# Optimization experiments

Hardware: AMD Instinct MI355X
Metric: run time of the kernel (lower is better)

The kernel has to match this reference:

```python
import jax, jax.numpy as jnp
import numpy as np

N = 100000
E = 1600000
IN_DIM, HID, Z = 128, 64, 32


def gcn_conv(x, src, dst, num_nodes, W, b):
    """PyG GCNConv: add self-loops, symmetric deg^-1/2 normalization.
    x: [N, F_in]; src/dst: [E] int (self-loops already appended by caller wrapper).
    """
    h = x @ W  # [N, F_out] transform first (PyG order)
    ones = jnp.ones(src.shape[0], dtype=x.dtype)
    deg = jax.ops.segment_sum(ones, dst, num_segments=num_nodes)  # in-degree incl. self-loop
    dinv = jnp.where(deg > 0, jax.lax.rsqrt(deg), 0.0)
    norm = dinv[src] * dinv[dst]  # [E]
    msgs = h[src] * norm[:, None]  # [E, F_out] irregular gather
    out = jax.ops.segment_sum(msgs, dst, num_segments=num_nodes)  # scatter-add
    return out + b


def setup_inputs() -> dict:
    key = jax.random.key(0)
    ks = jax.random.split(key, 10)
    x = jax.random.normal(ks[0], (N, IN_DIM), dtype=jnp.float32)
    edge_index = jax.random.randint(ks[1], (2, E), 0, N, dtype=jnp.int64)

    def glorot(k, fan_in, fan_out):
        s = jnp.sqrt(6.0 / (fan_in + fan_out))
        return jax.random.uniform(k, (fan_in, fan_out), jnp.float32, -s, s)

    return {
        "x": x,
        "edge_index": edge_index,
        "W1": glorot(ks[2], IN_DIM, HID),
        "b1": jnp.zeros((HID,), jnp.float32),
        "W2": glorot(ks[3], HID, Z),
        "b2": jnp.zeros((Z,), jnp.float32),
        "Wmu": glorot(ks[4], Z, Z),
        "bmu": jnp.zeros((Z,), jnp.float32),
        "Wlv": glorot(ks[5], Z, Z),
        "blv": jnp.zeros((Z,), jnp.float32),
    }


def reference(x, edge_index, W1, b1, W2, b2, Wmu, bmu, Wlv, blv):
    num_nodes = x.shape[0]
    loop = jnp.arange(num_nodes, dtype=edge_index.dtype)
    src = jnp.concatenate([edge_index[0], loop])  # self-loops appended
    dst = jnp.concatenate([edge_index[1], loop])
    h = jax.nn.relu(gcn_conv(x, src, dst, num_nodes, W1, b1))
    h = gcn_conv(h, src, dst, num_nodes, W2, b2)
    mu = h @ Wmu + bmu
    logvar = h @ Wlv + blv
    return (mu, logvar)
```

## Files before the change

kernel.cpp:

```cpp
#include <hip/hip_runtime.h>

#define N_NODES 100000
#define N_EDGES 1600000
#define IN_F   128
#define HID_F  64
#define Z_F    32
#define NBUK   782
#define BCAP   3072
#define P1T    4096
#define P1_BLOCKS ((N_EDGES + P1T - 1) / P1T)
#define AGG_CAP 2048
#define G1_BLOCKS ((N_NODES + 63) / 64)

typedef unsigned int uint32;
typedef __attribute__((ext_vector_type(8))) short bf16x8;
typedef __attribute__((ext_vector_type(4))) float f32x4;

__device__ __forceinline__ unsigned short f2bf(float f) {
    unsigned u = __float_as_uint(f);
    u = (u + 0x7FFF + ((u >> 16) & 1)) >> 16;
    return (unsigned short)u;
}
__device__ __forceinline__ uint32 pack2bf(float lo, float hi) {
    return (uint32)f2bf(lo) | ((uint32)f2bf(hi) << 16);
}
__device__ __forceinline__ float bflo(uint32 u) { return __uint_as_float(u << 16); }
__device__ __forceinline__ float bfhi(uint32 u) { return __uint_as_float(u & 0xFFFF0000u); }

#define ACC8(u) { a0 += bflo(u.x); a1 += bfhi(u.x); a2 += bflo(u.y); a3 += bfhi(u.y); \
                  a4 += bflo(u.z); a5 += bfhi(u.z); a6 += bflo(u.w); a7 += bfhi(u.w); }

__global__ __launch_bounds__(512) void phase1_kernel(const int* __restrict__ ei,
                                                     int* __restrict__ gcur,
                                                     uint32* __restrict__ pairs,
                                                     const float* __restrict__ W1,
                                                     const float* __restrict__ W2,
                                                     const float* __restrict__ Wmu,
                                                     const float* __restrict__ Wlv,
                                                     unsigned short* __restrict__ Wt1,
                                                     unsigned short* __restrict__ Wt2,
                                                     unsigned short* __restrict__ Wth) {
    if (blockIdx.x == P1_BLOCKS) {
        int t = threadIdx.x;
        for (int i = t; i < IN_F * HID_F; i += 512) {
            int n = i >> 7, k = i & 127;
            Wt1[i] = f2bf(W1[k * HID_F + n]);
        }
        for (int i = t; i < HID_F * Z_F; i += 512) {
            int n = i >> 6, k = i & 63;
            Wt2[i] = f2bf(W2[k * Z_F + n]);
        }
        for (int i = t; i < Z_F * 64; i += 512) {
            int n = i >> 5, k = i & 31;
            Wth[i] = f2bf(n < 32 ? Wmu[k * Z_F + n] : Wlv[k * Z_F + (n - 32)]);
        }
        return;
    }
    __shared__ int hist[NBUK];
    __shared__ int lbase[NBUK];
    __shared__ int gbase[NBUK];
    __shared__ int lcur[NBUK];
    __shared__ uint32 stage[P1T];
    __shared__ unsigned short sbid[P1T];
    __shared__ int part[512];
    int tid = threadIdx.x;
    int e0 = blockIdx.x * P1T;
    int ecnt = N_EDGES - e0; if (ecnt > P1T) ecnt = P1T;
    for (int b = tid; b < NBUK; b += 512) { hist[b] = 0; lcur[b] = 0; }
    __syncthreads();
    int myd[8];
#pragma unroll
    for (int i = 0; i < 8; i++) {
        int k = tid + i * 512;
        myd[i] = (k < ecnt) ? ei[N_EDGES + e0 + k] : -1;
    }
#pragma unroll
    for (int i = 0; i < 8; i++)
        if (myd[i] >= 0) atomicAdd(&hist[myd[i] >> 7], 1);
    __syncthreads();
    int t2 = tid * 2;
    int l0 = 0, l1 = 0, s = 0;
    if (t2 + 0 < NBUK) { l0 = hist[t2 + 0]; s += l0; }
    if (t2 + 1 < NBUK) { l1 = hist[t2 + 1]; s += l1; }
    part[tid] = s;
    __syncthreads();
    for (int off = 1; off < 512; off <<= 1) {
        int add = (tid >= off) ? part[tid - off] : 0;
        __syncthreads();
        part[tid] += add;
        __syncthreads();
    }
    int run = part[tid] - s;
    if (t2 + 0 < NBUK) { lbase[t2 + 0] = run; run += l0; }
    if (t2 + 1 < NBUK) { lbase[t2 + 1] = run; }
    for (int b = tid; b < NBUK; b += 512) {
        int h = hist[b];
        gbase[b] = h ? atomicAdd(&gcur[b], h) : 0;
    }
    __syncthreads();
#pragma unroll
    for (int i = 0; i < 8; i++) {
        int k = tid + i * 512;
        if (k < ecnt) {
            int sN = ei[e0 + k];
            int d  = myd[i];
            int b = d >> 7;
            int slot = lbase[b] + atomicAdd(&lcur[b], 1);
            stage[slot] = (uint32)sN | ((uint32)(d & 127) << 17);
            sbid[slot] = (unsigned short)b;
        }
    }
    __syncthreads();
    for (int k = tid; k < ecnt; k += 512) {
        int b = sbid[k];
        int r = gbase[b] + (k - lbase[k < ecnt ? b : 0]);
        r = gbase[b] + (k - lbase[b]);
        if (r < BCAP) pairs[(size_t)b * BCAP + r] = stage[k];
    }
}

__global__ __launch_bounds__(256) void p2g1_kernel(const uint32* __restrict__ pairs,
                                                   const int* __restrict__ gcur,
                                                   int* __restrict__ rowptr,
                                                   float* __restrict__ dinv,
                                                   int* __restrict__ col,
                                                   const float* __restrict__ x,
                                                   const unsigned short* __restrict__ Wt1,
                                                   unsigned short* __restrict__ t1) {
    int tid = threadIdx.x;
    if (blockIdx.x < NBUK) {
        __shared__ int lhist[128];
        __shared__ int lscan[128];
        __shared__ int lcur[128];
        __shared__ int stage[BCAP];
        __shared__ int wsum[4];
        int b = blockIdx.x;
        int cnt_b = gcur[b];
        if (cnt_b > BCAP) cnt_b = BCAP;
        int partial = 0;
        for (int i = tid; i < b; i += 256) partial += gcur[i];
#pragma unroll
        for (int off = 32; off > 0; off >>= 1) partial += __shfl_down(partial, off);
        if (tid < 128) { lhist[tid] = 0; lcur[tid] = 0; }
        if ((tid & 63) == 0) wsum[tid >> 6] = partial;
        __syncthreads();
        int gbase = wsum[0] + wsum[1] + wsum[2] + wsum[3];
        int node0 = b << 7;
        int nb = N_NODES - node0;
        if (nb > 128) nb = 128;
        const uint32* pb = pairs + (size_t)b * BCAP;
        for (int k = tid; k < cnt_b; k += 256) atomicAdd(&lhist[pb[k] >> 17], 1);
        __syncthreads();
        int v = (tid < 128) ? lhist[tid] : 0;
        if (tid < 128) lscan[tid] = v;
        __syncthreads();
        for (int off = 1; off < 128; off <<= 1) {
            int add = (tid < 128 && tid >= off) ? lscan[tid - off] : 0;
            __syncthreads();
            if (tid < 128) lscan[tid] += add;
            __syncthreads();
        }
        if (tid < 128) lscan[tid] -= v;
        __syncthreads();
        if (tid < nb) {
            rowptr[node0 + tid] = gbase + lscan[tid];
            dinv[node0 + tid] = rsqrtf((float)(lhist[tid] + 1));
        }
        if (b == NBUK - 1 && tid == 0) rowptr[N_NODES] = N_EDGES;
        for (int k = tid; k < cnt_b; k += 256) {
            uint32 u = pb[k];
            int ld = u >> 17;
            int r = atomicAdd(&lcur[ld], 1);
            stage[lscan[ld] + r] = (int)(u & 0x1FFFF);
        }
        __syncthreads();
        for (int k = tid; k < cnt_b; k += 256) col[gbase + k] = stage[k];
        return;
    }
    __shared__ unsigned short Cs[64 * 72];
    __shared__ float dv[64];
    __shared__ int h64[64];
    int g = blockIdx.x - NBUK;
    int node0 = g * 64;
    int bk = node0 >> 7, half = (node0 >> 6) & 1;
    int cnt_b = gcur[bk];
    if (cnt_b > BCAP) cnt_b = BCAP;
    if (tid < 64) h64[tid] = 0;
    __syncthreads();
    const uint32* pb = pairs + (size_t)bk * BCAP;
    for (int k = tid; k < cnt_b; k += 256) {
        int ld = pb[k] >> 17;
        if ((ld >> 6) == half) atomicAdd(&h64[ld & 63], 1);
    }
    __syncthreads();
    if (tid < 64) {
        int n = node0 + tid;
        dv[tid] = (n < N_NODES) ? rsqrtf((float)(h64[tid] + 1)) : 0.f;
    }
    __syncthreads();
    int w = tid >> 6, lane = tid & 63;
    int m = lane & 15, quad = lane >> 4;
    int row = w * 16 + m;
    int node = node0 + row;
    const float* xr = x + (size_t)min(node, N_NODES - 1) * IN_F;
    f32x4 acc0 = {0.f, 0.f, 0.f, 0.f};
    f32x4 acc1 = acc0, acc2 = acc0, acc3 = acc0;
#pragma unroll
    for (int ks = 0; ks < 4; ks++) {
        int kb = ks * 32 + quad * 8;
        float4 f0 = *(const float4*)(xr + kb);
        float4 f1 = *(const float4*)(xr + kb + 4);
        union { bf16x8 v; unsigned short u[8]; } A;
        A.u[0] = f2bf(f0.x); A.u[1] = f2bf(f0.y); A.u[2] = f2bf(f0.z); A.u[3] = f2bf(f0.w);
        A.u[4] = f2bf(f1.x); A.u[5] = f2bf(f1.y); A.u[6] = f2bf(f1.z); A.u[7] = f2bf(f1.w);
        bf16x8 b0 = *(const bf16x8*)&Wt1[(0 * 16 + m) * IN_F + kb];
        bf16x8 b1 = *(const bf16x8*)&Wt1[(1 * 16 + m) * IN_F + kb];
        bf16x8 b2 = *(const bf16x8*)&Wt1[(2 * 16 + m) * IN_F + kb];
        bf16x8 b3 = *(const bf16x8*)&Wt1[(3 * 16 + m) * IN_F + kb];
        acc0 = __builtin_amdgcn_mfma_f32_16x16x32_bf16(A.v, b0, acc0, 0, 0, 0);
        acc1 = __builtin_amdgcn_mfma_f32_16x16x32_bf16(A.v, b1, acc1, 0, 0, 0);
        acc2 = __builtin_amdgcn_mfma_f32_16x16x32_bf16(A.v, b2, acc2, 0, 0, 0);
        acc3 = __builtin_amdgcn_mfma_f32_16x16x32_bf16(A.v, b3, acc3, 0, 0, 0);
    }
    int rbase = w * 16 + quad * 4;
#pragma unroll
    for (int reg = 0; reg < 4; reg++) {
        int r = rbase + reg;
        float d = dv[r];
        Cs[r * 72 +  0 + m] = f2bf(acc0[reg] * d);
        Cs[r * 72 + 16 + m] = f2bf(acc1[reg] * d);
        Cs[r * 72 + 32 + m] = f2bf(acc2[reg] * d);
        Cs[r * 72 + 48 + m] = f2bf(acc3[reg] * d);
    }
    __syncthreads();
#pragma unroll
    for (int it = 0; it < 4; it++) {
        int idx = it * 256 + tid;
        int r = idx >> 4, c = idx & 15;
        int nd = node0 + r;
        if (nd < N_NODES) {
            uint2 vv = *(const uint2*)&Cs[r * 72 + c * 4];
            *(uint2*)&t1[(size_t)nd * HID_F + c * 4] = vv;
        }
    }
}

__global__ __launch_bounds__(256) void agg1gemm2_kernel(const unsigned short* __restrict__ t1,
                                                        const int* __restrict__ rowptr,
                                                        const int* __restrict__ col,
                                                        const float* __restrict__ dinv,
                                                        const float* __restrict__ b1,
                                                        const unsigned short* __restrict__ Wt2,
                                                        unsigned short* __restrict__ t2s) {
    __shared__ int lcol[AGG_CAP];
    __shared__ int lrp[65];
    __shared__ float ldv[64];
    __shared__ unsigned short h1s[64 * 72];
    __shared__ unsigned short Cs[64 * 36];
    int tid = threadIdx.x;
    int node0 = blockIdx.x * 64;
    if (tid < 65) lrp[tid] = rowptr[min(node0 + tid, N_NODES)];
    __syncthreads();
    int s0 = lrp[0];
    int cnt = lrp[64] - s0; if (cnt > AGG_CAP) cnt = AGG_CAP;
    for (int k = tid; k < cnt; k += 256) lcol[k] = col[s0 + k];
    if (tid < 64) {
        int n = node0 + tid;
        ldv[tid] = (n < N_NODES) ? dinv[n] : 0.f;
    }
    __syncthreads();
    int lane = tid & 63, w = tid >> 6;
    int grp = lane >> 3, fl = lane & 7;
    int gg = w * 8 + grp;
    const uint4* t1q = (const uint4*)t1;
    float4 bb0 = ((const float4*)b1)[fl * 2];
    float4 bb1 = ((const float4*)b1)[fl * 2 + 1];
#pragma unroll
    for (int rep = 0; rep < 2; rep++) {
        int li = gg + rep * 32;
        int node = node0 + li;
        uint4 pk = make_uint4(0u, 0u, 0u, 0u);
        if (node < N_NODES) {
            int s = lrp[li] - s0;
            int e = lrp[li + 1] - s0; if (e > cnt) e = cnt;
            float a0 = 0.f, a1 = 0.f, a2 = 0.f, a3 = 0.f;
            float a4 = 0.f, a5 = 0.f, a6 = 0.f, a7 = 0.f;
            int p = s;
            for (; p + 3 < e; p += 4) {
                int c0 = lcol[p], c1 = lcol[p + 1], c2 = lcol[p + 2], c3 = lcol[p + 3];
                uint4 u0 = t1q[(size_t)c0 * 8 + fl];
                uint4 u1 = t1q[(size_t)c1 * 8 + fl];
                uint4 u2 = t1q[(size_t)c2 * 8 + fl];
                uint4 u3 = t1q[(size_t)c3 * 8 + fl];
                ACC8(u0); ACC8(u1); ACC8(u2); ACC8(u3);
            }
            for (; p < e; p++) {
                uint4 u = t1q[(size_t)lcol[p] * 8 + fl];
                ACC8(u);
            }
            uint4 us = t1q[(size_t)node * 8 + fl];
            float di = ldv[li];
            float o0 = fmaxf(di * (a0 + bflo(us.x)) + bb0.x, 0.f);
            float o1 = fmaxf(di * (a1 + bfhi(us.x)) + bb0.y, 0.f);
            float o2 = fmaxf(di * (a2 + bflo(us.y)) + bb0.z, 0.f);
            float o3 = fmaxf(di * (a3 + bfhi(us.y)) + bb0.w, 0.f);
            float o4 = fmaxf(di * (a4 + bflo(us.z)) + bb1.x, 0.f);
            float o5 = fmaxf(di * (a5 + bfhi(us.z)) + bb1.y, 0.f);
            float o6 = fmaxf(di * (a6 + bflo(us.w)) + bb1.z, 0.f);
            float o7 = fmaxf(di * (a7 + bfhi(us.w)) + bb1.w, 0.f);
            pk.x = pack2bf(o0, o1);
            pk.y = pack2bf(o2, o3);
            pk.z = pack2bf(o4, o5);
            pk.w = pack2bf(o6, o7);
        }
        *(uint4*)&h1s[li * 72 + fl * 8] = pk;
    }
    __syncthreads();
    int m = lane & 15, quad = lane >> 4;
    int row = w * 16 + m;
    f32x4 acc0 = {0.f, 0.f, 0.f, 0.f};
    f32x4 acc1 = acc0;
#pragma unroll
    for (int ks = 0; ks < 2; ks++) {
        int kb = ks * 32 + quad * 8;
        bf16x8 a  = *(const bf16x8*)&h1s[row * 72 + kb];
        bf16x8 b0 = *(const bf16x8*)&Wt2[(0 * 16 + m) * HID_F + kb];
        bf16x8 b1v = *(const bf16x8*)&Wt2[(1 * 16 + m) * HID_F + kb];
        acc0 = __builtin_amdgcn_mfma_f32_16x16x32_bf16(a, b0, acc0, 0, 0, 0);
        acc1 = __builtin_amdgcn_mfma_f32_16x16x32_bf16(a, b1v, acc1, 0, 0, 0);
    }
    int rbase = w * 16 + quad * 4;
#pragma unroll
    for (int reg = 0; reg < 4; reg++) {
        int r = rbase + reg;
        float d = ldv[r];
        Cs[r * 36 +  0 + m] = f2bf(acc0[reg] * d);
        Cs[r * 36 + 16 + m] = f2bf(acc1[reg] * d);
    }
    __syncthreads();
#pragma unroll
    for (int it = 0; it < 2; it++) {
        int idx = it * 256 + tid;
        int r = idx >> 3, c = idx & 7;
        int nd = node0 + r;
        if (nd < N_NODES) {
            uint2 vv = *(const uint2*)&Cs[r * 36 + c * 4];
            *(uint2*)&t2s[(size_t)nd * Z_F + c * 4] = vv;
        }
    }
}

__global__ __launch_bounds__(256) void agg2heads_kernel(const unsigned short* __restrict__ t2s,
                                                        const int* __restrict__ rowptr,
                                                        const int* __restrict__ col,
                                                        const float* __restrict__ dinv,
                                                        const float* __restrict__ b2,
                                                        const unsigned short* __restrict__ Wth,
                                                        const float* __restrict__ bmu,
                                                        const float* __restrict__ blv,
                                                        float* __restrict__ out) {
    __shared__ int lcol[AGG_CAP];
    __shared__ int lrp[65];
    __shared__ float ldv[64];
    __shared__ unsigned short h2s[64 * 40];
    __shared__ float Cf[64 * 68];
    __shared__ float bias[64];
    int tid = threadIdx.x;
    int node0 = blockIdx.x * 64;
    if (tid < 65) lrp[tid] = rowptr[min(node0 + tid, N_NODES)];
    else if (tid >= 96 && tid < 128) bias[tid - 96] = bmu[tid - 96];
    else if (tid >= 128 && tid < 160) bias[tid - 96] = blv[tid - 128];
    __syncthreads();
    int s0 = lrp[0];
    int cnt = lrp[64] - s0; if (cnt > AGG_CAP) cnt = AGG_CAP;
    for (int k = tid; k < cnt; k += 256) lcol[k] = col[s0 + k];
    if (tid < 64) {
        int n = node0 + tid;
        ldv[tid] = (n < N_NODES) ? dinv[n] : 0.f;
    }
    __syncthreads();
    int lane = tid & 63, w = tid >> 6;
    int grp = lane >> 2, fo = lane & 3;
    int li = w * 16 + grp;
    const uint4* t2q = (const uint4*)t2s;
    float4 bb0 = ((const float4*)b2)[fo * 2];
    float4 bb1 = ((const float4*)b2)[fo * 2 + 1];
    {
        int node = node0 + li;
        uint4 pk = make_uint4(0u, 0u, 0u, 0u);
        if (node < N_NODES) {
            int s = lrp[li] - s0;
            int e = lrp[li + 1] - s0; if (e > cnt) e = cnt;
            float a0 = 0.f, a1 = 0.f, a2 = 0.f, a3 = 0.f;
            float a4 = 0.f, a5 = 0.f, a6 = 0.f, a7 = 0.f;
            int p = s;
            for (; p + 3 < e; p += 4) {
                int c0 = lcol[p], c1 = lcol[p + 1], c2 = lcol[p + 2], c3 = lcol[p + 3];
                uint4 u0 = t2q[(size_t)c0 * 4 + fo];
                uint4 u1 = t2q[(size_t)c1 * 4 + fo];
                uint4 u2 = t2q[(size_t)c2 * 4 + fo];
                uint4 u3 = t2q[(size_t)c3 * 4 + fo];
                ACC8(u0); ACC8(u1); ACC8(u2); ACC8(u3);
            }
            for (; p < e; p++) {
                uint4 u = t2q[(size_t)lcol[p] * 4 + fo];
                ACC8(u);
            }
            uint4 us = t2q[(size_t)node * 4 + fo];
            float di = ldv[li];
            float o0 = di * (a0 + bflo(us.x)) + bb0.x;
            float o1 = di * (a1 + bfhi(us.x)) + bb0.y;
            float o2 = di * (a2 + bflo(us.y)) + bb0.z;
            float o3 = di * (a3 + bfhi(us.y)) + bb0.w;
            float o4 = di * (a4 + bflo(us.z)) + bb1.x;
            float o5 = di * (a5 + bfhi(us.z)) + bb1.y;
            float o6 = di * (a6 + bflo(us.w)) + bb1.z;
            float o7 = di * (a7 + bfhi(us.w)) + bb1.w;
            pk.x = pack2bf(o0, o1);
            pk.y = pack2bf(o2, o3);
            pk.z = pack2bf(o4, o5);
            pk.w = pack2bf(o6, o7);
        }
        *(uint4*)&h2s[li * 40 + fo * 8] = pk;
    }
    __syncthreads();
    int m = lane & 15, quad = lane >> 4;
    int row = w * 16 + m;
    int kb = quad * 8;
    bf16x8 a  = *(const bf16x8*)&h2s[row * 40 + kb];
    bf16x8 b0 = *(const bf16x8*)&Wth[(0 * 16 + m) * Z_F + kb];
    bf16x8 b1 = *(const bf16x8*)&Wth[(1 * 16 + m) * Z_F + kb];
    bf16x8 b2v = *(const bf16x8*)&Wth[(2 * 16 + m) * Z_F + kb];
    bf16x8 b3 = *(const bf16x8*)&Wth[(3 * 16 + m) * Z_F + kb];
    f32x4 acc0 = {0.f, 0.f, 0.f, 0.f};
    f32x4 acc1 = acc0, acc2 = acc0, acc3 = acc0;
    acc0 = __builtin_amdgcn_mfma_f32_16x16x32_bf16(a, b0, acc0, 0, 0, 0);
    acc1 = __builtin_amdgcn_mfma_f32_16x16x32_bf16(a, b1, acc1, 0, 0, 0);
    acc2 = __builtin_amdgcn_mfma_f32_16x16x32_bf16(a, b2v, acc2, 0, 0, 0);
    acc3 = __builtin_amdgcn_mfma_f32_16x16x32_bf16(a, b3, acc3, 0, 0, 0);
    int rbase = w * 16 + quad * 4;
#pragma unroll
    for (int reg = 0; reg < 4; reg++) {
        int r = rbase + reg;
        Cf[r * 68 +  0 + m] = acc0[reg] + bias[ 0 + m];
        Cf[r * 68 + 16 + m] = acc1[reg] + bias[16 + m];
        Cf[r * 68 + 32 + m] = acc2[reg] + bias[32 + m];
        Cf[r * 68 + 48 + m] = acc3[reg] + bias[48 + m];
    }
    __syncthreads();
#pragma unroll
    for (int it = 0; it < 2; it++) {
        int idx = it * 256 + tid;
        int r = idx >> 3, c = idx & 7;
        int nd = node0 + r;
        if (nd < N_NODES) {
            float4 vmu = *(const float4*)&Cf[r * 68 + c * 4];
            float4 vlv = *(const float4*)&Cf[r * 68 + 32 + c * 4];
            *(float4*)&out[(size_t)nd * Z_F + c * 4] = vmu;
            *(float4*)&out[(size_t)N_NODES * Z_F + (size_t)nd * Z_F + c * 4] = vlv;
        }
    }
}

extern "C" void kernel_launch(void* const* d_in, const int* in_sizes, int n_in,
                              void* d_out, int out_size, void* d_ws, size_t ws_size,
                              hipStream_t stream) {
    const float* x   = (const float*)d_in[0];
    const int*   ei  = (const int*)d_in[1];
    const float* W1  = (const float*)d_in[2];
    const float* b1  = (const float*)d_in[3];
    const float* W2  = (const float*)d_in[4];
    const float* b2  = (const float*)d_in[5];
    const float* Wmu = (const float*)d_in[6];
    const float* bmu = (const float*)d_in[7];
    const float* Wlv = (const float*)d_in[8];
    const float* blv = (const float*)d_in[9];
    float* out = (float*)d_out;

    char* ws = (char*)d_ws;
    size_t off = 0;
    auto A = [&](size_t bytes) {
        size_t r = off;
        off += (bytes + 255) & ~(size_t)255;
        return r;
    };
    int*   gcur   = (int*)(ws + A((size_t)NBUK * 4));
    int*   rowptr = (int*)(ws + A((size_t)(N_NODES + 1) * 4));
    float* dinv   = (float*)(ws + A((size_t)N_NODES * 4));
    unsigned short* Wt1 = (unsigned short*)(ws + A((size_t)IN_F * HID_F * 2));
    unsigned short* Wt2 = (unsigned short*)(ws + A((size_t)HID_F * Z_F * 2));
    unsigned short* Wth = (unsigned short*)(ws + A((size_t)Z_F * 64 * 2));
    int*   col        = (int*)(ws + A((size_t)N_EDGES * 4));
    char*  reg1 = ws + A((size_t)NBUK * BCAP * 4);
    uint32* pairs = (uint32*)reg1;
    unsigned short* t2s = (unsigned short*)reg1;
    unsigned short* t1 = (unsigned short*)(ws + A((size_t)N_NODES * HID_F * 2));

    hipMemsetAsync(gcur, 0, (size_t)NBUK * 4, stream);

    phase1_kernel<<<P1_BLOCKS + 1, 512, 0, stream>>>(ei, gcur, pairs,
                                                     W1, W2, Wmu, Wlv, Wt1, Wt2, Wth);
    p2g1_kernel<<<NBUK + G1_BLOCKS, 256, 0, stream>>>(pairs, gcur, rowptr, dinv, col,
                                                      x, Wt1, t1);
    agg1gemm2_kernel<<<G1_BLOCKS, 256, 0, stream>>>(t1, rowptr, col, dinv, b1, Wt2, t2s);
    agg2heads_kernel<<<G1_BLOCKS, 256, 0, stream>>>(t2s, rowptr, col, dinv, b2, Wth, bmu, blv, out);
}
```

Before: 210.6 us.

## Degree-sort aggregation rows and widen second aggregation to 128 nodes per block

Both aggregation kernels now rank the nodes in a block by degree and pair the heaviest row with the lightest across the two reps, so lanes carry more even gather work. The second aggregation kernel handles 128 nodes per block, which halves its grid, and writes the MFMA head results straight to global memory instead of staging them in shared memory first. The per-block rank sort costs O(n^2) shared-memory reads. The direct stores are narrower and less coalesced, and the larger edge cap raises shared-memory use.

New measurement: 217.3 us. 1.03x slower.

```diff
diff --git a/kernel.cpp b/kernel.cpp
--- a/kernel.cpp
+++ b/kernel.cpp
@@ -10,6 +10,7 @@
 #define P1T    4096
 #define P1_BLOCKS ((N_EDGES + P1T - 1) / P1T)
 #define AGG_CAP 2048
+#define A2_CAP  3072
 #define G1_BLOCKS ((N_NODES + 63) / 64)
 
 typedef unsigned int uint32;
@@ -113,8 +114,7 @@
     __syncthreads();
     for (int k = tid; k < ecnt; k += 512) {
         int b = sbid[k];
-        int r = gbase[b] + (k - lbase[k < ecnt ? b : 0]);
-        r = gbase[b] + (k - lbase[b]);
+        int r = gbase[b] + (k - lbase[b]);
         if (r < BCAP) pairs[(size_t)b * BCAP + r] = stage[k];
     }
 }
@@ -255,6 +255,7 @@
     __shared__ int lcol[AGG_CAP];
     __shared__ int lrp[65];
     __shared__ float ldv[64];
+    __shared__ int ord[64];
     __shared__ unsigned short h1s[64 * 72];
     __shared__ unsigned short Cs[64 * 36];
     int tid = threadIdx.x;
@@ -267,6 +268,13 @@
     if (tid < 64) {
         int n = node0 + tid;
         ldv[tid] = (n < N_NODES) ? dinv[n] : 0.f;
+        int di = lrp[tid + 1] - lrp[tid];
+        int r = 0;
+        for (int j = 0; j < 64; j++) {
+            int dj = lrp[j + 1] - lrp[j];
+            r += (dj > di) || (dj == di && j < tid);
+        }
+        ord[r] = tid;
     }
     __syncthreads();
     int lane = tid & 63, w = tid >> 6;
@@ -277,7 +285,7 @@
     float4 bb1 = ((const float4*)b1)[fl * 2 + 1];
 #pragma unroll
     for (int rep = 0; rep < 2; rep++) {
-        int li = gg + rep * 32;
+        int li = rep ? ord[63 - gg] : ord[gg];
         int node = node0 + li;
         uint4 pk = make_uint4(0u, 0u, 0u, 0u);
         if (node < N_NODES) {
@@ -313,7 +321,8 @@
             pk.z = pack2bf(o4, o5);
             pk.w = pack2bf(o6, o7);
         }
-        *(uint4*)&h1s[li * 72 + fl * 8] = pk;
+        int sli = rep ? ord[63 - gg] : ord[gg];
+        *(uint4*)&h1s[sli * 72 + fl * 8] = pk;
     }
     __syncthreads();
     int m = lane & 15, quad = lane >> 4;
@@ -359,33 +368,42 @@
                                                         const float* __restrict__ bmu,
                                                         const float* __restrict__ blv,
                                                         float* __restrict__ out) {
-    __shared__ int lcol[AGG_CAP];
-    __shared__ int lrp[65];
-    __shared__ float ldv[64];
-    __shared__ unsigned short h2s[64 * 40];
-    __shared__ float Cf[64 * 68];
+    __shared__ int lcol[A2_CAP];
+    __shared__ int lrp[129];
+    __shared__ float ldv[128];
+    __shared__ int ord[128];
+    __shared__ unsigned short h2s[128 * 40];
     __shared__ float bias[64];
     int tid = threadIdx.x;
-    int node0 = blockIdx.x * 64;
-    if (tid < 65) lrp[tid] = rowptr[min(node0 + tid, N_NODES)];
-    else if (tid >= 96 && tid < 128) bias[tid - 96] = bmu[tid - 96];
-    else if (tid >= 128 && tid < 160) bias[tid - 96] = blv[tid - 128];
+    int node0 = blockIdx.x * 128;
+    if (tid < 129) lrp[tid] = rowptr[min(node0 + tid, N_NODES)];
+    else if (tid >= 160 && tid < 192) bias[tid - 160] = bmu[tid - 160];
+    else if (tid >= 192 && tid < 224) bias[tid - 160] = blv[tid - 192];
     __syncthreads();
     int s0 = lrp[0];
-    int cnt = lrp[64] - s0; if (cnt > AGG_CAP) cnt = AGG_CAP;
+    int cnt = lrp[128] - s0; if (cnt > A2_CAP) cnt = A2_CAP;
     for (int k = tid; k < cnt; k += 256) lcol[k] = col[s0 + k];
-    if (tid < 64) {
+    if (tid < 128) {
         int n = node0 + tid;
         ldv[tid] = (n < N_NODES) ? dinv[n] : 0.f;
+        int di = lrp[tid + 1] - lrp[tid];
+        int r = 0;
+        for (int j = 0; j < 128; j++) {
+            int dj = lrp[j + 1] - lrp[j];
+            r += (dj > di) || (dj == di && j < tid);
+        }
+        ord[r] = tid;
     }
     __syncthreads();
     int lane = tid & 63, w = tid >> 6;
     int grp = lane >> 2, fo = lane & 3;
-    int li = w * 16 + grp;
+    int g = w * 16 + grp;
     const uint4* t2q = (const uint4*)t2s;
     float4 bb0 = ((const float4*)b2)[fo * 2];
     float4 bb1 = ((const float4*)b2)[fo * 2 + 1];
-    {
+#pragma unroll
+    for (int rep = 0; rep < 2; rep++) {
+        int li = rep ? ord[127 - g] : ord[g];
         int node = node0 + li;
         uint4 pk = make_uint4(0u, 0u, 0u, 0u);
         if (node < N_NODES) {
@@ -425,39 +443,32 @@
     }
     __syncthreads();
     int m = lane & 15, quad = lane >> 4;
-    int row = w * 16 + m;
     int kb = quad * 8;
-    bf16x8 a  = *(const bf16x8*)&h2s[row * 40 + kb];
-    bf16x8 b0 = *(const bf16x8*)&Wth[(0 * 16 + m) * Z_F + kb];
-    bf16x8 b1 = *(const bf16x8*)&Wth[(1 * 16 + m) * Z_F + kb];
-    bf16x8 b2v = *(const bf16x8*)&Wth[(2 * 16 + m) * Z_F + kb];
-    bf16x8 b3 = *(const bf16x8*)&Wth[(3 * 16 + m) * Z_F + kb];
-    f32x4 acc0 = {0.f, 0.f, 0.f, 0.f};
-    f32x4 acc1 = acc0, acc2 = acc0, acc3 = acc0;
-    acc0 = __builtin_amdgcn_mfma_f32_16x16x32_bf16(a, b0, acc0, 0, 0, 0);
-    acc1 = __builtin_amdgcn_mfma_f32_16x16x32_bf16(a, b1, acc1, 0, 0, 0);
-    acc2 = __builtin_amdgcn_mfma_f32_16x16x32_bf16(a, b2v, acc2, 0, 0, 0);
-    acc3 = __builtin_amdgcn_mfma_f32_16x16x32_bf16(a, b3, acc3, 0, 0, 0);
-    int rbase = w * 16 + quad * 4;
-#pragma unroll
-    for (int reg = 0; reg < 4; reg++) {
-        int r = rbase + reg;
-        Cf[r * 68 +  0 + m] = acc0[reg] + bias[ 0 + m];
-        Cf[r * 68 + 16 + m] = acc1[reg] + bias[16 + m];
-        Cf[r * 68 + 32 + m] = acc2[reg] + bias[32 + m];
-        Cf[r * 68 + 48 + m] = acc3[reg] + bias[48 + m];
-    }
-    __syncthreads();
-#pragma unroll
-    for (int it = 0; it < 2; it++) {
-        int idx = it * 256 + tid;
-        int r = idx >> 3, c = idx & 7;
-        int nd = node0 + r;
-        if (nd < N_NODES) {
-            float4 vmu = *(const float4*)&Cf[r * 68 + c * 4];
-            float4 vlv = *(const float4*)&Cf[r * 68 + 32 + c * 4];
-            *(float4*)&out[(size_t)nd * Z_F + c * 4] = vmu;
-            *(float4*)&out[(size_t)N_NODES * Z_F + (size_t)nd * Z_F + c * 4] = vlv;
+    float* outlv = out + (size_t)N_NODES * Z_F;
+#pragma unroll
+    for (int rt = 0; rt < 2; rt++) {
+        int row = w * 32 + rt * 16 + m;
+        bf16x8 a  = *(const bf16x8*)&h2s[row * 40 + kb];
+        bf16x8 B0 = *(const bf16x8*)&Wth[(0 * 16 + m) * Z_F + kb];
+        bf16x8 B1 = *(const bf16x8*)&Wth[(1 * 16 + m) * Z_F + kb];
+        bf16x8 B2 = *(const bf16x8*)&Wth[(2 * 16 + m) * Z_F + kb];
+        bf16x8 B3 = *(const bf16x8*)&Wth[(3 * 16 + m) * Z_F + kb];
+        f32x4 acc0 = {0.f, 0.f, 0.f, 0.f};
+        f32x4 acc1 = acc0, acc2 = acc0, acc3 = acc0;
+        acc0 = __builtin_amdgcn_mfma_f32_16x16x32_bf16(a, B0, acc0, 0, 0, 0);
+        acc1 = __builtin_amdgcn_mfma_f32_16x16x32_bf16(a, B1, acc1, 0, 0, 0);
+        acc2 = __builtin_amdgcn_mfma_f32_16x16x32_bf16(a, B2, acc2, 0, 0, 0);
+        acc3 = __builtin_amdgcn_mfma_f32_16x16x32_bf16(a, B3, acc3, 0, 0, 0);
+#pragma unroll
+        for (int reg = 0; reg < 4; reg++) {
+            int r = w * 32 + rt * 16 + quad * 4 + reg;
+            int nd = node0 + r;
+            if (nd < N_NODES) {
+                out[(size_t)nd * Z_F +  0 + m]   = acc0[reg] + bias[ 0 + m];
+                out[(size_t)nd * Z_F + 16 + m]   = acc1[reg] + bias[16 + m];
+                outlv[(size_t)nd * Z_F +  0 + m] = acc2[reg] + bias[32 + m];
+                outlv[(size_t)nd * Z_F + 16 + m] = acc3[reg] + bias[48 + m];
+            }
         }
     }
 }
@@ -503,5 +514,5 @@
     p2g1_kernel<<<NBUK + G1_BLOCKS, 256, 0, stream>>>(pairs, gcur, rowptr, dinv, col,
                                                       x, Wt1, t1);
     agg1gemm2_kernel<<<G1_BLOCKS, 256, 0, stream>>>(t1, rowptr, col, dinv, b1, Wt2, t2s);
-    agg2heads_kernel<<<G1_BLOCKS, 256, 0, stream>>>(t2s, rowptr, col, dinv, b2, Wth, bmu, blv, out);
-}
+    agg2heads_kernel<<<NBUK, 256, 0, stream>>>(t2s, rowptr, col, dinv, b2, Wth, bmu, blv, out);
+}
```
